# Kernel tuning notes

Measured on AMD Instinct MI355X. Metric: run time of the kernel, lower is better.

The kernel has to match this reference:

```python
import jax, jax.numpy as jnp
import numpy as np

NUM_HEADS = 16
HEAD_DIM = 64  # hidden 1024 / 16


def setup_inputs() -> dict:
    key = jax.random.key(0)
    k1, k2, k3 = jax.random.split(key, 3)
    B, S, H = 2, 2048, 1024
    return {
        "hidden_states": jax.random.normal(k1, (B, S, H), dtype=jnp.float32),
        "attention_mask": jnp.zeros((B, 1, 1, S), dtype=jnp.float32),
        "c_attn_w": jax.random.normal(k2, (H, 3 * H), dtype=jnp.float32) * 0.02,
        "c_attn_b": jnp.zeros((3 * H,), dtype=jnp.float32),
        "c_proj_w": jax.random.normal(k3, (H, H), dtype=jnp.float32) * 0.02,
        "c_proj_b": jnp.zeros((H,), dtype=jnp.float32),
    }


def reference(hidden_states, attention_mask, c_attn_w, c_attn_b, c_proj_w, c_proj_b):
    B, S, H = hidden_states.shape
    nH, hd = NUM_HEADS, HEAD_DIM
    # Conv1D: x @ w + b (HF weight layout is (in, out))
    qkv = hidden_states @ c_attn_w + c_attn_b  # [B,S,3H]
    q, k, v = jnp.split(qkv, 3, axis=-1)
    # split heads -> [B,nH,S,hd]
    def heads(t):
        return t.reshape(B, S, nH, hd).transpose(0, 2, 1, 3)
    q, k, v = heads(q), heads(k), heads(v)
    scores = jnp.einsum("bhqd,bhkd->bhqk", q, k) / np.sqrt(hd).astype(jnp.float32)
    scores = scores + attention_mask  # additive mask, broadcast [B,1,1,S]
    attn = jax.nn.softmax(scores, axis=-1)  # dropout is identity (eval)
    ctx = jnp.einsum("bhqk,bhkd->bhqd", attn, v)
    ctx = ctx.transpose(0, 2, 1, 3).reshape(B, S, H)  # merge heads
    out = ctx @ c_proj_w + c_proj_b
    return out
```

## Files before the change

kernel.cpp:

```cpp
#include <hip/hip_runtime.h>
#include <hip/hip_bf16.h>

typedef __attribute__((ext_vector_type(8))) short short8;
typedef __attribute__((ext_vector_type(4))) float f32x4;

__device__ __forceinline__ unsigned short f2bf(float f) {
  union { __hip_bfloat16 h; unsigned short u; } cv;
  cv.h = __float2bfloat16(f);
  return cv.u;
}

__device__ __forceinline__ void gld16(const void* g, void* l) {
  __builtin_amdgcn_global_load_lds(
      (const __attribute__((address_space(1))) unsigned int*)g,
      (__attribute__((address_space(3))) unsigned int*)l, 16, 0, 0);
}

__device__ __forceinline__ f32x4 mfma_bf16(short8 a, short8 b, f32x4 c) {
  return __builtin_amdgcn_mfma_f32_16x16x32_bf16(a, b, c, 0, 0, 0);
}

#define QSCALE 0.18033688011112042f
#define L2E    1.4426950408889634f

__global__ void prep(const float* __restrict__ x, unsigned short* __restrict__ xbf,
                     const float* __restrict__ wa, unsigned short* __restrict__ da,
                     const float* __restrict__ wp, unsigned short* __restrict__ dp) {
  __shared__ float tile[64][65];
  const int t = threadIdx.x;
  const int bid = blockIdx.x;
  if (bid < 4096) {
    int i = bid * 256 + t;
    float4 v = ((const float4*)x)[i];
    ushort4 o;
    o.x = f2bf(v.x); o.y = f2bf(v.y); o.z = f2bf(v.z); o.w = f2bf(v.w);
    ((ushort4*)xbf)[i] = o;
    return;
  }
  int idx = bid - 4096;
  const int tr = idx & 15;
  int y = idx >> 4;
  const float* src;
  unsigned short* dst;
  int C;
  if (y < 48) { src = wa; dst = da; C = 3072; }
  else        { src = wp; dst = dp; C = 1024; y -= 48; }
  const int tc = y;
#pragma unroll
  for (int i = 0; i < 16; ++i) {
    int id2 = t + i * 256;
    int lr = id2 >> 6, lc = id2 & 63;
    tile[lr][lc] = src[(size_t)(tr * 64 + lr) * C + tc * 64 + lc];
  }
  __syncthreads();
#pragma unroll
  for (int i = 0; i < 16; ++i) {
    int id2 = t + i * 256;
    int lr = id2 >> 6, lc = id2 & 63;
    dst[(size_t)(tc * 64 + lr) * 1024 + tr * 64 + lc] = f2bf(tile[lc][lr]);
  }
}

template <int KDIM>
__device__ __forceinline__ void gemm_core(const short* __restrict__ A, const short* __restrict__ Bt,
                                          int mbase, int nbase, short* As, short* Bs,
                                          int wm, int wn, int quad, int l16, int t,
                                          f32x4 (&acc)[4][4]) {
  for (int kt = 0; kt < KDIM / 32; ++kt) {
#pragma unroll
    for (int i = 0; i < 2; ++i) {
      int c = t + i * 256;
      int row = c >> 2, c4 = c & 3;
      gld16(A + (size_t)(mbase + row) * KDIM + kt * 32 + c4 * 8, (char*)As + c * 16);
      gld16(Bt + (size_t)(nbase + row) * KDIM + kt * 32 + c4 * 8, (char*)Bs + c * 16);
    }
    __syncthreads();
    short8 af[4], bf[4];
#pragma unroll
    for (int m = 0; m < 4; ++m)
      af[m] = *(const short8*)((const char*)As + (wm + m * 16 + l16) * 64 + quad * 16);
#pragma unroll
    for (int n = 0; n < 4; ++n)
      bf[n] = *(const short8*)((const char*)Bs + (wn + n * 16 + l16) * 64 + quad * 16);
#pragma unroll
    for (int m = 0; m < 4; ++m)
#pragma unroll
      for (int n = 0; n < 4; ++n)
        acc[m][n] = mfma_bf16(af[m], bf[n], acc[m][n]);
    __syncthreads();
  }
}

__global__ __launch_bounds__(256, 2) void gemm_qkv(
    const short* __restrict__ A, const short* __restrict__ Bt, const float* __restrict__ bias,
    unsigned short* __restrict__ q, unsigned short* __restrict__ k,
    unsigned short* __restrict__ vt) {
  __shared__ __align__(16) char smem[17408];
  short* As = (short*)smem;
  short* Bs = (short*)(smem + 8192);
  unsigned short* vlds = (unsigned short*)smem;
  const int t = threadIdx.x;
  const int wave = t >> 6, lane = t & 63;
  const int quad = lane >> 4, l16 = lane & 15;
  const int wm = (wave >> 1) * 64, wn = (wave & 1) * 64;
  const int mbase = blockIdx.x * 128, nbase = blockIdx.y * 128;
  f32x4 acc[4][4];
#pragma unroll
  for (int i = 0; i < 4; ++i)
#pragma unroll
    for (int j = 0; j < 4; ++j) acc[i][j] = (f32x4)0.0f;
  gemm_core<1024>(A, Bt, mbase, nbase, As, Bs, wm, wn, quad, l16, t, acc);

  if (nbase < 2048) {
#pragma unroll
    for (int n = 0; n < 4; ++n) {
      int col = nbase + wn + n * 16 + l16;
      float bc = bias[col];
      int which = col >> 10, rem = col & 1023;
      int h = rem >> 6, d = rem & 63;
      unsigned short* dst = which ? k : q;
      float scale = which ? 1.0f : QSCALE;
#pragma unroll
      for (int m = 0; m < 4; ++m) {
#pragma unroll
        for (int r = 0; r < 4; ++r) {
          int row = mbase + wm + m * 16 + quad * 4 + r;
          int b = row >> 11, s = row & 2047;
          dst[(((size_t)(b * 16 + h)) * 2048 + s) * 64 + d] = f2bf((acc[m][n][r] + bc) * scale);
        }
      }
    }
  } else {
    const int b = mbase >> 11, s0 = mbase & 2047;
    const int vcb = nbase - 2048;
    __syncthreads();
#pragma unroll
    for (int half = 0; half < 2; ++half) {
      if (wn == half * 64) {
#pragma unroll
        for (int n = 0; n < 4; ++n) {
          int col_l = n * 16 + l16;
          float bc = bias[nbase + half * 64 + col_l];
#pragma unroll
          for (int m = 0; m < 4; ++m)
#pragma unroll
            for (int r = 0; r < 4; ++r) {
              int row_l = wm + m * 16 + quad * 4 + r;
              vlds[col_l * 136 + ((row_l & 15) * 8 + (row_l >> 4))] = f2bf(acc[m][n][r] + bc);
            }
        }
      }
      __syncthreads();
      int h = (vcb + half * 64) >> 6;
      size_t obase = ((size_t)(b * 16 + h)) * 64 * 2048;
#pragma unroll
      for (int i = 0; i < 4; ++i) {
        int c = t + i * 256;
        int d_l = c >> 4, c16 = c & 15;
        short8 v = *(const short8*)&vlds[d_l * 136 + c16 * 8];
        *(short8*)&vt[obase + (size_t)d_l * 2048 + s0 + c16 * 8] = v;
      }
      __syncthreads();
    }
  }
}

__global__ __launch_bounds__(256, 2) void gemm_proj(
    const short* __restrict__ A, const short* __restrict__ Bt, const float* __restrict__ bias,
    float* __restrict__ out) {
  __shared__ __align__(16) short As[64 * 32];
  __shared__ __align__(16) short Bs[128 * 32];
  const int t = threadIdx.x;
  const int wave = t >> 6, lane = t & 63;
  const int quad = lane >> 4, l16 = lane & 15;
  const int wm = (wave >> 1) * 32, wn = (wave & 1) * 64;
  const int mbase = blockIdx.x * 64, nbase = blockIdx.y * 128;
  f32x4 acc[2][4];
#pragma unroll
  for (int i = 0; i < 2; ++i)
#pragma unroll
    for (int j = 0; j < 4; ++j) acc[i][j] = (f32x4)0.0f;
  for (int kt = 0; kt < 32; ++kt) {
    {
      int row = t >> 2, c4 = t & 3;
      gld16(A + (size_t)(mbase + row) * 1024 + kt * 32 + c4 * 8, (char*)As + t * 16);
    }
#pragma unroll
    for (int i = 0; i < 2; ++i) {
      int c = t + i * 256;
      int row = c >> 2, c4 = c & 3;
      gld16(Bt + (size_t)(nbase + row) * 1024 + kt * 32 + c4 * 8, (char*)Bs + c * 16);
    }
    __syncthreads();
    short8 af[2], bf[4];
#pragma unroll
    for (int m = 0; m < 2; ++m)
      af[m] = *(const short8*)((const char*)As + (wm + m * 16 + l16) * 64 + quad * 16);
#pragma unroll
    for (int n = 0; n < 4; ++n)
      bf[n] = *(const short8*)((const char*)Bs + (wn + n * 16 + l16) * 64 + quad * 16);
#pragma unroll
    for (int m = 0; m < 2; ++m)
#pragma unroll
      for (int n = 0; n < 4; ++n)
        acc[m][n] = mfma_bf16(af[m], bf[n], acc[m][n]);
    __syncthreads();
  }
#pragma unroll
  for (int n = 0; n < 4; ++n) {
    int col = nbase + wn + n * 16 + l16;
    float bc = bias[col];
#pragma unroll
    for (int m = 0; m < 2; ++m)
#pragma unroll
      for (int r = 0; r < 4; ++r) {
        int row = mbase + wm + m * 16 + quad * 4 + r;
        out[(size_t)row * 1024 + col] = acc[m][n][r] + bc;
      }
  }
}

__global__ __launch_bounds__(128, 2) void flash_attn(
    const short* __restrict__ Qg, const short* __restrict__ Kg, const short* __restrict__ Vtg,
    const float* __restrict__ mask, unsigned short* __restrict__ ctx) {
  __shared__ __align__(16) unsigned char smem[40960];
  short* Psm = (short*)(smem + 32768);
  const int t = threadIdx.x;
  const int wave = t >> 6, lane = t & 63;
  const int quad = lane >> 4, l16 = lane & 15;
  const int bh = blockIdx.x, b = bh >> 4, h = bh & 15;
  const int qbase = blockIdx.y * 64;
  const size_t bh_off = (size_t)bh * 2048 * 64;

#pragma unroll
  for (int i = 0; i < 4; ++i) {
    int c = t + i * 128;
    int row = c >> 3, col = c & 7;
    gld16(Qg + bh_off + (size_t)(qbase + row) * 64 + (col ^ (row & 7)) * 8,
          (char*)smem + c * 16);
  }
  __syncthreads();
  short8 qf[2][2];
#pragma unroll
  for (int m = 0; m < 2; ++m)
#pragma unroll
    for (int ks = 0; ks < 2; ++ks) {
      int row = wave * 32 + m * 16 + l16;
      qf[m][ks] = *(const short8*)((const char*)smem +
                                   (row * 8 + ((ks * 4 + quad) ^ (l16 & 7))) * 16);
    }
  __syncthreads();

  auto stage_k = [&](char* dst, int kn) {
#pragma unroll
    for (int i = 0; i < 8; ++i) {
      int c = t + i * 128;
      int row = c >> 3, col = c & 7;
      gld16(Kg + bh_off + (size_t)(kn * 128 + row) * 64 + (col ^ (row & 7)) * 8,
            dst + c * 16);
    }
  };

  f32x4 O[2][4];
  float l_i[2][4];
#pragma unroll
  for (int m = 0; m < 2; ++m)
#pragma unroll
    for (int d = 0; d < 4; ++d) O[m][d] = (f32x4)0.0f;
#pragma unroll
  for (int m = 0; m < 2; ++m)
#pragma unroll
    for (int r = 0; r < 4; ++r) l_i[m][r] = 0.0f;

  stage_k((char*)smem, 0);
  __syncthreads();

  for (int kt = 0; kt < 16; ++kt) {
    const char* Kc = (const char*)smem + (kt & 1) * 16384;
    char* Kn = (char*)smem + ((kt + 1) & 1) * 16384;

    float mv[8];
#pragma unroll
    for (int n = 0; n < 8; ++n) mv[n] = mask[b * 2048 + kt * 128 + n * 16 + l16];

    short8 vfc[4][4];
#pragma unroll
    for (int ks = 0; ks < 4; ++ks)
#pragma unroll
      for (int db = 0; db < 4; ++db)
        vfc[ks][db] = *(const short8*)(Vtg + ((size_t)bh * 64 + db * 16 + l16) * 2048 +
                                       kt * 128 + (ks * 4 + quad) * 8);

    if (kt < 15) stage_k(Kn, kt + 1);

    f32x4 sa[2][8];
#pragma unroll
    for (int m = 0; m < 2; ++m)
#pragma unroll
      for (int n = 0; n < 8; ++n) sa[m][n] = (f32x4)0.0f;
    __builtin_amdgcn_s_setprio(1);
#pragma unroll
    for (int ks = 0; ks < 2; ++ks) {
#pragma unroll
      for (int n = 0; n < 8; ++n) {
        int row = n * 16 + l16;
        short8 kf = *(const short8*)(Kc + (row * 8 + ((ks * 4 + quad) ^ (l16 & 7))) * 16);
        sa[0][n] = mfma_bf16(qf[0][ks], kf, sa[0][n]);
        sa[1][n] = mfma_bf16(qf[1][ks], kf, sa[1][n]);
      }
    }
    __builtin_amdgcn_s_setprio(0);

#pragma unroll
    for (int m = 0; m < 2; ++m) {
#pragma unroll
      for (int r = 0; r < 4; ++r) {
        float rs = 0.0f;
        short8 p8;
#pragma unroll
        for (int n = 0; n < 8; ++n) {
          float p = __builtin_amdgcn_exp2f(__builtin_fmaf(mv[n], L2E, sa[m][n][r]));
          rs += p;
          p8[n] = (short)f2bf(p);
        }
        int prow = wave * 16 + quad * 4 + r;
        *(short8*)((char*)Psm + prow * 256 + ((l16 ^ (prow & 7)) * 16)) = p8;
        l_i[m][r] += rs;
      }
      asm volatile("" ::: "memory");

      __builtin_amdgcn_s_setprio(1);
#pragma unroll
      for (int ks = 0; ks < 4; ++ks) {
        int prow = wave * 16 + l16;
        short8 pf = *(const short8*)((const char*)Psm +
                                     prow * 256 + (((ks * 4 + quad) ^ (l16 & 7)) * 16));
#pragma unroll
        for (int db = 0; db < 4; ++db)
          O[m][db] = mfma_bf16(pf, vfc[ks][db], O[m][db]);
      }
      __builtin_amdgcn_s_setprio(0);
      asm volatile("" ::: "memory");
    }
    __syncthreads();
  }

#pragma unroll
  for (int m = 0; m < 2; ++m) {
#pragma unroll
    for (int r = 0; r < 4; ++r) {
      float l = l_i[m][r];
      l += __shfl_xor(l, 1);
      l += __shfl_xor(l, 2);
      l += __shfl_xor(l, 4);
      l += __shfl_xor(l, 8);
      float inv = 1.0f / l;
      int s = qbase + wave * 32 + m * 16 + quad * 4 + r;
      size_t o = ((size_t)b * 2048 + s) * 1024 + h * 64;
#pragma unroll
      for (int db = 0; db < 4; ++db)
        ctx[o + db * 16 + l16] = f2bf(O[m][db][r] * inv);
    }
  }
}

extern "C" void kernel_launch(void* const* d_in, const int* in_sizes, int n_in,
                              void* d_out, int out_size, void* d_ws, size_t ws_size,
                              hipStream_t stream) {
  const float* x      = (const float*)d_in[0];
  const float* mask   = (const float*)d_in[1];
  const float* w_attn = (const float*)d_in[2];
  const float* b_attn = (const float*)d_in[3];
  const float* w_proj = (const float*)d_in[4];
  const float* b_proj = (const float*)d_in[5];
  float* out = (float*)d_out;

  char* ws = (char*)d_ws;
  const size_t MB = 1024 * 1024;
  short*          Xbf    = (short*)(ws);
  short*          Wqkv_t = (short*)(ws + 8 * MB);
  short*          Wprj_t = (short*)(ws + 14 * MB);
  unsigned short* Qb     = (unsigned short*)(ws + 16 * MB);
  unsigned short* Kb     = (unsigned short*)(ws + 24 * MB);
  unsigned short* Vtb    = (unsigned short*)(ws + 32 * MB);
  unsigned short* ctx    = (unsigned short*)Xbf;

  prep<<<5120, 256, 0, stream>>>(x, (unsigned short*)Xbf,
                                 w_attn, (unsigned short*)Wqkv_t,
                                 w_proj, (unsigned short*)Wprj_t);
  gemm_qkv<<<dim3(32, 24), 256, 0, stream>>>(Xbf, Wqkv_t, b_attn, Qb, Kb, Vtb);
  flash_attn<<<dim3(32, 32), 128, 0, stream>>>((const short*)Qb, (const short*)Kb,
                                               (const short*)Vtb, mask, ctx);
  gemm_proj<<<dim3(64, 8), 256, 0, stream>>>((const short*)ctx, Wprj_t, b_proj, out);
}
```

Baseline: 219.0 us.

## Restructure flash attention into 4-wave blocks with LDS-staged double-buffered K/V tiles

The attention kernel moves to 256-thread blocks where each wave owns 16 query rows, and the key loop now walks 64-key tiles instead of 128. V tiles are no longer read straight from global memory into registers. They are staged into shared memory alongside K with async global-to-LDS loads and double buffering. The V-transpose epilogue in the QKV GEMM reorders its LDS write index so the stored layout matches the new 64-key tile ordering. This aims to raise occupancy, cut per-thread register pressure, and remove strided global V loads, at the cost of twice as many loop iterations and barriers.

```diff
diff --git a/kernel.cpp b/kernel.cpp
--- a/kernel.cpp
+++ b/kernel.cpp
@@ -2,6 +2,7 @@
 #include <hip/hip_bf16.h>
 
 typedef __attribute__((ext_vector_type(8))) short short8;
+typedef __attribute__((ext_vector_type(4))) short short4v;
 typedef __attribute__((ext_vector_type(4))) float f32x4;
 
 __device__ __forceinline__ unsigned short f2bf(float f) {
@@ -146,7 +147,8 @@
 #pragma unroll
             for (int r = 0; r < 4; ++r) {
               int row_l = wm + m * 16 + quad * 4 + r;
-              vlds[col_l * 136 + ((row_l & 15) * 8 + (row_l >> 4))] = f2bf(acc[m][n][r] + bc);
+              int idx = (row_l & 64) + (row_l & 15) * 4 + ((row_l >> 4) & 3);
+              vlds[col_l * 136 + idx] = f2bf(acc[m][n][r] + bc);
             }
         }
       }
@@ -220,7 +222,7 @@
   }
 }
 
-__global__ __launch_bounds__(128, 2) void flash_attn(
+__global__ __launch_bounds__(256, 4) void flash_attn(
     const short* __restrict__ Qg, const short* __restrict__ Kg, const short* __restrict__ Vtg,
     const float* __restrict__ mask, unsigned short* __restrict__ ctx) {
   __shared__ __align__(16) unsigned char smem[40960];
@@ -233,134 +235,119 @@
   const size_t bh_off = (size_t)bh * 2048 * 64;
 
 #pragma unroll
-  for (int i = 0; i < 4; ++i) {
-    int c = t + i * 128;
+  for (int i = 0; i < 2; ++i) {
+    int c = t + i * 256;
     int row = c >> 3, col = c & 7;
     gld16(Qg + bh_off + (size_t)(qbase + row) * 64 + (col ^ (row & 7)) * 8,
           (char*)smem + c * 16);
   }
   __syncthreads();
-  short8 qf[2][2];
-#pragma unroll
-  for (int m = 0; m < 2; ++m)
+  short8 qf[2];
+#pragma unroll
+  for (int ks = 0; ks < 2; ++ks) {
+    int row = wave * 16 + l16;
+    qf[ks] = *(const short8*)((const char*)smem +
+                              (row * 8 + ((ks * 4 + quad) ^ (l16 & 7))) * 16);
+  }
+  __syncthreads();
+
+  auto stage = [&](int kn) {
+    char* kd = (char*)smem + (kn & 1) * 8192;
+    char* vd = (char*)smem + 16384 + (kn & 1) * 8192;
+#pragma unroll
+    for (int i = 0; i < 2; ++i) {
+      int c = t + i * 256;
+      int row = c >> 3, col = c & 7;
+      gld16(Kg + bh_off + (size_t)(kn * 64 + row) * 64 + (col ^ (row & 7)) * 8,
+            kd + c * 16);
+      gld16(Vtg + ((size_t)bh * 64 + row) * 2048 + kn * 64 + (col ^ (row & 7)) * 8,
+            vd + c * 16);
+    }
+  };
+
+  f32x4 O[4];
+  float l_i[4];
+#pragma unroll
+  for (int d = 0; d < 4; ++d) O[d] = (f32x4)0.0f;
+#pragma unroll
+  for (int r = 0; r < 4; ++r) l_i[r] = 0.0f;
+
+  stage(0);
+  __syncthreads();
+
+  for (int kt = 0; kt < 32; ++kt) {
+    const char* Kc = (const char*)smem + (kt & 1) * 8192;
+    const char* Vc = (const char*)smem + 16384 + (kt & 1) * 8192;
+
+    float mv[4];
+#pragma unroll
+    for (int n = 0; n < 4; ++n) mv[n] = mask[b * 2048 + kt * 64 + n * 16 + l16];
+
+    if (kt < 31) stage(kt + 1);
+
+    f32x4 sa[4];
+#pragma unroll
+    for (int n = 0; n < 4; ++n) sa[n] = (f32x4)0.0f;
+    __builtin_amdgcn_s_setprio(1);
 #pragma unroll
     for (int ks = 0; ks < 2; ++ks) {
-      int row = wave * 32 + m * 16 + l16;
-      qf[m][ks] = *(const short8*)((const char*)smem +
-                                   (row * 8 + ((ks * 4 + quad) ^ (l16 & 7))) * 16);
-    }
-  __syncthreads();
-
-  auto stage_k = [&](char* dst, int kn) {
-#pragma unroll
-    for (int i = 0; i < 8; ++i) {
-      int c = t + i * 128;
-      int row = c >> 3, col = c & 7;
-      gld16(Kg + bh_off + (size_t)(kn * 128 + row) * 64 + (col ^ (row & 7)) * 8,
-            dst + c * 16);
-    }
-  };
-
-  f32x4 O[2][4];
-  float l_i[2][4];
-#pragma unroll
-  for (int m = 0; m < 2; ++m)
-#pragma unroll
-    for (int d = 0; d < 4; ++d) O[m][d] = (f32x4)0.0f;
-#pragma unroll
-  for (int m = 0; m < 2; ++m)
-#pragma unroll
-    for (int r = 0; r < 4; ++r) l_i[m][r] = 0.0f;
-
-  stage_k((char*)smem, 0);
-  __syncthreads();
-
-  for (int kt = 0; kt < 16; ++kt) {
-    const char* Kc = (const char*)smem + (kt & 1) * 16384;
-    char* Kn = (char*)smem + ((kt + 1) & 1) * 16384;
-
-    float mv[8];
-#pragma unroll
-    for (int n = 0; n < 8; ++n) mv[n] = mask[b * 2048 + kt * 128 + n * 16 + l16];
-
-    short8 vfc[4][4];
-#pragma unroll
-    for (int ks = 0; ks < 4; ++ks)
-#pragma unroll
-      for (int db = 0; db < 4; ++db)
-        vfc[ks][db] = *(const short8*)(Vtg + ((size_t)bh * 64 + db * 16 + l16) * 2048 +
-                                       kt * 128 + (ks * 4 + quad) * 8);
-
-    if (kt < 15) stage_k(Kn, kt + 1);
-
-    f32x4 sa[2][8];
-#pragma unroll
-    for (int m = 0; m < 2; ++m)
-#pragma unroll
-      for (int n = 0; n < 8; ++n) sa[m][n] = (f32x4)0.0f;
-    __builtin_amdgcn_s_setprio(1);
-#pragma unroll
-    for (int ks = 0; ks < 2; ++ks) {
-#pragma unroll
-      for (int n = 0; n < 8; ++n) {
+#pragma unroll
+      for (int n = 0; n < 4; ++n) {
         int row = n * 16 + l16;
         short8 kf = *(const short8*)(Kc + (row * 8 + ((ks * 4 + quad) ^ (l16 & 7))) * 16);
-        sa[0][n] = mfma_bf16(qf[0][ks], kf, sa[0][n]);
-        sa[1][n] = mfma_bf16(qf[1][ks], kf, sa[1][n]);
+        sa[n] = mfma_bf16(qf[ks], kf, sa[n]);
       }
     }
     __builtin_amdgcn_s_setprio(0);
 
 #pragma unroll
-    for (int m = 0; m < 2; ++m) {
-#pragma unroll
-      for (int r = 0; r < 4; ++r) {
-        float rs = 0.0f;
-        short8 p8;
-#pragma unroll
-        for (int n = 0; n < 8; ++n) {
-          float p = __builtin_amdgcn_exp2f(__builtin_fmaf(mv[n], L2E, sa[m][n][r]));
-          rs += p;
-          p8[n] = (short)f2bf(p);
-        }
-        int prow = wave * 16 + quad * 4 + r;
-        *(short8*)((char*)Psm + prow * 256 + ((l16 ^ (prow & 7)) * 16)) = p8;
-        l_i[m][r] += rs;
-      }
-      asm volatile("" ::: "memory");
-
-      __builtin_amdgcn_s_setprio(1);
-#pragma unroll
-      for (int ks = 0; ks < 4; ++ks) {
-        int prow = wave * 16 + l16;
-        short8 pf = *(const short8*)((const char*)Psm +
-                                     prow * 256 + (((ks * 4 + quad) ^ (l16 & 7)) * 16));
-#pragma unroll
-        for (int db = 0; db < 4; ++db)
-          O[m][db] = mfma_bf16(pf, vfc[ks][db], O[m][db]);
-      }
-      __builtin_amdgcn_s_setprio(0);
-      asm volatile("" ::: "memory");
-    }
-    __syncthreads();
-  }
-
-#pragma unroll
-  for (int m = 0; m < 2; ++m) {
-#pragma unroll
     for (int r = 0; r < 4; ++r) {
-      float l = l_i[m][r];
-      l += __shfl_xor(l, 1);
-      l += __shfl_xor(l, 2);
-      l += __shfl_xor(l, 4);
-      l += __shfl_xor(l, 8);
-      float inv = 1.0f / l;
-      int s = qbase + wave * 32 + m * 16 + quad * 4 + r;
-      size_t o = ((size_t)b * 2048 + s) * 1024 + h * 64;
-#pragma unroll
-      for (int db = 0; db < 4; ++db)
-        ctx[o + db * 16 + l16] = f2bf(O[m][db][r] * inv);
-    }
+      float rs = 0.0f;
+      short4v p4;
+#pragma unroll
+      for (int n = 0; n < 4; ++n) {
+        float p = __builtin_amdgcn_exp2f(__builtin_fmaf(mv[n], L2E, sa[n][r]));
+        rs += p;
+        p4[n] = (short)f2bf(p);
+      }
+      int prow = wave * 16 + quad * 4 + r;
+      *(short4v*)((char*)Psm + prow * 128 +
+                  (((l16 >> 1) ^ (prow & 7)) * 16) + (l16 & 1) * 8) = p4;
+      l_i[r] += rs;
+    }
+    asm volatile("" ::: "memory");
+
+    __builtin_amdgcn_s_setprio(1);
+#pragma unroll
+    for (int ks = 0; ks < 2; ++ks) {
+      int u = ks * 4 + quad;
+      int prow = wave * 16 + l16;
+      short8 pf = *(const short8*)((const char*)Psm + prow * 128 + ((u ^ (l16 & 7)) * 16));
+#pragma unroll
+      for (int db = 0; db < 4; ++db) {
+        int d = db * 16 + l16;
+        short8 vf = *(const short8*)(Vc + d * 128 + ((u ^ (d & 7)) * 16));
+        O[db] = mfma_bf16(pf, vf, O[db]);
+      }
+    }
+    __builtin_amdgcn_s_setprio(0);
+
+    __syncthreads();
+  }
+
+#pragma unroll
+  for (int r = 0; r < 4; ++r) {
+    float l = l_i[r];
+    l += __shfl_xor(l, 1);
+    l += __shfl_xor(l, 2);
+    l += __shfl_xor(l, 4);
+    l += __shfl_xor(l, 8);
+    float inv = 1.0f / l;
+    int s = qbase + wave * 16 + quad * 4 + r;
+    size_t o = ((size_t)b * 2048 + s) * 1024 + h * 64;
+#pragma unroll
+    for (int db = 0; db < 4; ++db)
+      ctx[o + db * 16 + l16] = f2bf(O[db][r] * inv);
   }
 }
 
@@ -389,7 +376,7 @@
                                  w_attn, (unsigned short*)Wqkv_t,
                                  w_proj, (unsigned short*)Wprj_t);
   gemm_qkv<<<dim3(32, 24), 256, 0, stream>>>(Xbf, Wqkv_t, b_attn, Qb, Kb, Vtb);
-  flash_attn<<<dim3(32, 32), 128, 0, stream>>>((const short*)Qb, (const short*)Kb,
+  flash_attn<<<dim3(32, 32), 256, 0, stream>>>((const short*)Qb, (const short*)Kb,
                                                (const short*)Vtb, mask, ctx);
   gemm_proj<<<dim3(64, 8), 256, 0, stream>>>((const short*)ctx, Wprj_t, b_proj, out);
 }
```

Measured after the change: 188.7 us. 13.9% less time.
